# Optimization experiments

Hardware: AMD Instinct MI355X
Metric: run time of the kernel (lower is better)

The kernel has to match this reference:

```python
import jax, jax.numpy as jnp
import numpy as np

BITS = 4
GROUPSIZE = 128
IN_F = 4096
OUT_F = 11008
VALS_PER_I32 = 32 // BITS  # 8
MASK = (1 << BITS) - 1     # 0xF


def _dequant_weight(qweight, qzeros, scales):
    """GPTQ 4-bit dequant. qweight: [K//8, N] int32 packed along K;
    qzeros: [G, N//8] int32 packed along N; scales: [G, N].
    Returns float32 weight [K, N]."""
    shifts = (jnp.arange(VALS_PER_I32, dtype=jnp.uint32) * BITS)
    # unpack weights: each int32 row holds 8 consecutive K-rows
    qw = qweight.astype(jnp.uint32)                              # [K//8, N]
    w_int = ((qw[:, None, :] >> shifts[None, :, None]) & MASK)   # [K//8, 8, N]
    w_int = w_int.reshape(IN_F, OUT_F)                           # [K, N]
    # unpack zeros: each int32 col holds 8 consecutive N-cols; stored zeros = z - 1
    qz = qzeros.astype(jnp.uint32)                               # [G, N//8]
    z_int = ((qz[:, :, None] >> shifts[None, None, :]) & MASK)   # [G, N//8, 8]
    n_groups = qzeros.shape[0]
    z_int = z_int.reshape(n_groups, OUT_F) + 1                   # [G, N]
    # per-group dequant: w = scales[g] * (q - z[g])
    g_idx = jnp.arange(IN_F) // GROUPSIZE                        # [K]
    w = (w_int.astype(jnp.float32) - z_int.astype(jnp.float32)[g_idx]) * scales[g_idx]
    return w                                                     # [K, N]


def setup_inputs() -> dict:
    key = jax.random.key(0)
    k1, k2, k3, k4, k5 = jax.random.split(key, 5)
    n_groups = IN_F // GROUPSIZE
    x = jax.random.normal(k1, (4, IN_F), dtype=jnp.float32)
    scales = jax.random.uniform(k2, (n_groups, OUT_F), dtype=jnp.float32,
                                minval=0.001, maxval=0.01)
    bias = jax.random.normal(k3, (OUT_F,), dtype=jnp.float32)
    qweight = jax.random.randint(k4, (IN_F // 32 * BITS, OUT_F), 0, 2147483647,
                                 dtype=jnp.int32)
    qzeros = jax.random.randint(k5, (n_groups, OUT_F // 256 * (BITS * 8)), 0,
                                2147483647, dtype=jnp.int32)
    return {"x": x, "scales": scales, "bias": bias,
            "qweight": qweight, "qzeros": qzeros}


def reference(x, scales, bias, qweight, qzeros):
    w = _dequant_weight(qweight, qzeros, scales)    # [K, N] float32
    y = x.astype(jnp.float32) @ w + bias            # [tokens, N]
    return y.astype(x.dtype)
```

## Files before the change

### kernel.cpp

```cpp
#include <hip/hip_runtime.h>

#define IN_F 4096
#define OUT_F 11008
#define GROUPSIZE 128
#define NGROUPS 32
#define QROWS 512
#define ZCOLS 1376
#define KSPLIT 8
#define WS_FLOATS (KSPLIT * 4 * OUT_F)

__global__ __launch_bounds__(256) void gptq_partial_kernel(
    const float* __restrict__ x,
    const float* __restrict__ scales,
    const int*   __restrict__ qweight,
    const int*   __restrict__ qzeros,
    float*       __restrict__ ws)
{
    __shared__ float part[4][4][64];

    const int tid = threadIdx.x;
    const int col = tid & 63;
    const int kp  = tid >> 6;
    const int n   = blockIdx.x * 64 + col;
    const int g   = blockIdx.y * 4 + kp;
    const int gu  = __builtin_amdgcn_readfirstlane(g);

    const unsigned qz = (unsigned)qzeros[g * ZCOLS + (n >> 3)];
    const float zf = (float)(((qz >> (4u * (unsigned)(n & 7))) & 0xFu) + 1u);
    const float sc = scales[g * OUT_F + n];

    float ga[4] = {0.f, 0.f, 0.f, 0.f};
    const int kkbase = gu * (GROUPSIZE / 8);

    #pragma unroll
    for (int t = 0; t < GROUPSIZE / 8; ++t) {
        const int kk = kkbase + t;
        const unsigned w = (unsigned)qweight[kk * OUT_F + n];
        const unsigned lo = w & 0x0F0F0F0Fu;
        const unsigned hi = (w >> 4) & 0x0F0F0F0Fu;
        float q[8];
        q[0] = (float)(lo & 0xFFu);
        q[1] = (float)(hi & 0xFFu);
        q[2] = (float)((lo >> 8) & 0xFFu);
        q[3] = (float)((hi >> 8) & 0xFFu);
        q[4] = (float)((lo >> 16) & 0xFFu);
        q[5] = (float)((hi >> 16) & 0xFFu);
        q[6] = (float)((lo >> 24) & 0xFFu);
        q[7] = (float)((hi >> 24) & 0xFFu);

        const int k0 = kk * 8;
        #pragma unroll
        for (int j = 0; j < 8; ++j) {
            const float d = q[j] - zf;
            #pragma unroll
            for (int m = 0; m < 4; ++m) ga[m] += x[m * IN_F + k0 + j] * d;
        }
    }

    #pragma unroll
    for (int m = 0; m < 4; ++m) part[kp][m][col] = sc * ga[m];
    __syncthreads();

    const int m = tid >> 6;
    const int c = tid & 63;
    const int nn = blockIdx.x * 64 + c;
    const float s = part[0][m][c] + part[1][m][c] + part[2][m][c] + part[3][m][c];
    ws[(blockIdx.y * 4 + m) * OUT_F + nn] = s;
}

__global__ __launch_bounds__(256) void gptq_reduce_kernel(
    const float* __restrict__ ws,
    const float* __restrict__ bias,
    float*       __restrict__ out)
{
    const int n = blockIdx.x * 256 + threadIdx.x;
    const int m = blockIdx.y;
    float s = bias[n];
    #pragma unroll
    for (int ks = 0; ks < KSPLIT; ++ks)
        s += ws[(ks * 4 + m) * OUT_F + n];
    out[m * OUT_F + n] = s;
}

__global__ __launch_bounds__(256) void gptq_gemv_fused(
    const float* __restrict__ x, const float* __restrict__ scales,
    const float* __restrict__ bias, const int* __restrict__ qweight,
    const int* __restrict__ qzeros, float* __restrict__ out)
{
    __shared__ float part[4][4][64];
    const int tid = threadIdx.x;
    const int col = tid & 63;
    const int kp  = tid >> 6;
    const int n   = blockIdx.x * 64 + col;
    const unsigned zshift = 4u * (unsigned)(n & 7);
    const int zcol = n >> 3;
    float acc[4] = {0.f, 0.f, 0.f, 0.f};
    const int g0 = kp * (NGROUPS / 4);
    for (int g = g0; g < g0 + NGROUPS / 4; ++g) {
        const unsigned qz = (unsigned)qzeros[g * ZCOLS + zcol];
        const float zf = (float)(((qz >> zshift) & 0xFu) + 1u);
        const float sc = scales[g * OUT_F + n];
        float ga[4] = {0.f, 0.f, 0.f, 0.f};
        const int kkbase = g * (GROUPSIZE / 8);
        #pragma unroll 4
        for (int t = 0; t < GROUPSIZE / 8; ++t) {
            const int kk = kkbase + t;
            const unsigned w = (unsigned)qweight[kk * OUT_F + n];
            const unsigned lo = w & 0x0F0F0F0Fu;
            const unsigned hi = (w >> 4) & 0x0F0F0F0Fu;
            float q[8];
            q[0] = (float)(lo & 0xFFu);         q[1] = (float)(hi & 0xFFu);
            q[2] = (float)((lo >> 8) & 0xFFu);  q[3] = (float)((hi >> 8) & 0xFFu);
            q[4] = (float)((lo >> 16) & 0xFFu); q[5] = (float)((hi >> 16) & 0xFFu);
            q[6] = (float)((lo >> 24) & 0xFFu); q[7] = (float)((hi >> 24) & 0xFFu);
            const int k0 = kk * 8;
            #pragma unroll
            for (int j = 0; j < 8; ++j) {
                const float d = q[j] - zf;
                #pragma unroll
                for (int m = 0; m < 4; ++m) acc[m] += x[m * IN_F + k0 + j] * d * sc;
            }
        }
        (void)0;
    }
    #pragma unroll
    for (int m = 0; m < 4; ++m) part[kp][m][col] = acc[m];
    __syncthreads();
    const int m = tid >> 6;
    const int c = tid & 63;
    const int nn = blockIdx.x * 64 + c;
    const float s = part[0][m][c] + part[1][m][c] + part[2][m][c] + part[3][m][c];
    out[m * OUT_F + nn] = s + bias[nn];
}

extern "C" void kernel_launch(void* const* d_in, const int* in_sizes, int n_in,
                              void* d_out, int out_size, void* d_ws, size_t ws_size,
                              hipStream_t stream) {
    const float* x       = (const float*)d_in[0];
    const float* scales  = (const float*)d_in[1];
    const float* bias    = (const float*)d_in[2];
    const int*   qweight = (const int*)d_in[3];
    const int*   qzeros  = (const int*)d_in[4];
    float*       out     = (float*)d_out;

    if (ws_size >= WS_FLOATS * sizeof(float)) {
        float* ws = (float*)d_ws;
        dim3 g1(OUT_F / 64, KSPLIT);
        gptq_partial_kernel<<<g1, 256, 0, stream>>>(x, scales, qweight, qzeros, ws);
        dim3 g2(OUT_F / 256, 4);
        gptq_reduce_kernel<<<g2, 256, 0, stream>>>(ws, bias, out);
    } else {
        dim3 grid(OUT_F / 64);
        gptq_gemv_fused<<<grid, 256, 0, stream>>>(x, scales, bias, qweight, qzeros, out);
    }
}
```

Baseline: 16.84 us.

## Split GPTQ GEMV per group with int4 vector loads and packed-float math

Adds a new first stage in which each thread handles 4 adjacent output columns via int4 qweight loads and float4 scales. Each block covers one quantization group, split four ways in K across its waves, and the inner math uses 2-wide float vectors to allow packed FMA. Partials for all 32 groups go to a larger workspace, which a second kernel reduces with four independent accumulators. The change trades wider loads and more K-parallelism for more workspace traffic and a longer reduction. It falls back to the old paths when the workspace is too small.

```diff
diff --git a/kernel.cpp b/kernel.cpp
--- a/kernel.cpp
+++ b/kernel.cpp
@@ -1,4 +1,6 @@
 #include <hip/hip_runtime.h>
+
+typedef float v2f __attribute__((ext_vector_type(2)));
 
 #define IN_F 4096
 #define OUT_F 11008
@@ -6,32 +8,134 @@
 #define NGROUPS 32
 #define QROWS 512
 #define ZCOLS 1376
-#define KSPLIT 8
-#define WS_FLOATS (KSPLIT * 4 * OUT_F)
-
-__global__ __launch_bounds__(256) void gptq_partial_kernel(
+#define WS_NEW_BYTES ((size_t)NGROUPS * 4 * OUT_F * sizeof(float))
+#define WS_OLD_BYTES ((size_t)8 * 4 * OUT_F * sizeof(float))
+
+__global__ __launch_bounds__(256) void gptq_s1(
     const float* __restrict__ x,
     const float* __restrict__ scales,
     const int*   __restrict__ qweight,
     const int*   __restrict__ qzeros,
     float*       __restrict__ ws)
 {
+    __shared__ float part[4][4][256];
+
+    const int tid  = threadIdx.x;
+    const int lane = tid & 63;
+    const int kq   = __builtin_amdgcn_readfirstlane(tid >> 6);
+    const int c0   = blockIdx.x * 256 + lane * 4;
+    const int g    = blockIdx.y;
+
+    const unsigned qz  = (unsigned)qzeros[g * ZCOLS + (c0 >> 3)];
+    const unsigned zsh = 4u * (unsigned)(c0 & 7);
+    v2f zz[4];
+    #pragma unroll
+    for (int c = 0; c < 4; ++c) {
+        const float zf = (float)(((qz >> (zsh + 4u * c)) & 0xFu) + 1u);
+        zz[c].x = zf; zz[c].y = zf;
+    }
+
+    const float4 sc4 = *(const float4*)(scales + g * OUT_F + c0);
+
+    const int row0 = g * 16 + kq * 4;
+    v2f acc[4][4] = {};
+
+    #pragma unroll
+    for (int t = 0; t < 4; ++t) {
+        const int row = row0 + t;
+        const int4 w4 = *(const int4*)(qweight + row * OUT_F + c0);
+        const int k0  = row * 8;
+
+        v2f xp[4][4];
+        #pragma unroll
+        for (int m = 0; m < 4; ++m)
+            #pragma unroll
+            for (int jj = 0; jj < 4; ++jj)
+                xp[m][jj] = *(const v2f*)(x + m * IN_F + k0 + 2 * jj);
+
+        const unsigned wv[4] = {(unsigned)w4.x, (unsigned)w4.y,
+                                (unsigned)w4.z, (unsigned)w4.w};
+        #pragma unroll
+        for (int c = 0; c < 4; ++c) {
+            const unsigned w  = wv[c];
+            const unsigned lo = w & 0x0F0F0F0Fu;
+            const unsigned hi = (w >> 4) & 0x0F0F0F0Fu;
+            v2f d[4];
+            d[0].x = (float)(lo & 0xFFu);         d[0].y = (float)(hi & 0xFFu);
+            d[1].x = (float)((lo >> 8) & 0xFFu);  d[1].y = (float)((hi >> 8) & 0xFFu);
+            d[2].x = (float)((lo >> 16) & 0xFFu); d[2].y = (float)((hi >> 16) & 0xFFu);
+            d[3].x = (float)(lo >> 24);           d[3].y = (float)(hi >> 24);
+            #pragma unroll
+            for (int jj = 0; jj < 4; ++jj) d[jj] = d[jj] - zz[c];
+            #pragma unroll
+            for (int m = 0; m < 4; ++m) {
+                acc[m][c] += xp[m][0] * d[0];
+                acc[m][c] += xp[m][1] * d[1];
+                acc[m][c] += xp[m][2] * d[2];
+                acc[m][c] += xp[m][3] * d[3];
+            }
+        }
+    }
+
+    #pragma unroll
+    for (int m = 0; m < 4; ++m) {
+        float4 r;
+        r.x = (acc[m][0].x + acc[m][0].y) * sc4.x;
+        r.y = (acc[m][1].x + acc[m][1].y) * sc4.y;
+        r.z = (acc[m][2].x + acc[m][2].y) * sc4.z;
+        r.w = (acc[m][3].x + acc[m][3].y) * sc4.w;
+        *(float4*)&part[kq][m][lane * 4] = r;
+    }
+    __syncthreads();
+
+    const int m  = tid >> 6;
+    const int cc = (tid & 63) * 4;
+    float4 a = *(const float4*)&part[0][m][cc];
+    const float4 b = *(const float4*)&part[1][m][cc];
+    const float4 c2 = *(const float4*)&part[2][m][cc];
+    const float4 d2 = *(const float4*)&part[3][m][cc];
+    a.x += b.x + c2.x + d2.x;
+    a.y += b.y + c2.y + d2.y;
+    a.z += b.z + c2.z + d2.z;
+    a.w += b.w + c2.w + d2.w;
+    *(float4*)(ws + (g * 4 + m) * OUT_F + blockIdx.x * 256 + cc) = a;
+}
+
+__global__ __launch_bounds__(256) void gptq_s2(
+    const float* __restrict__ ws,
+    const float* __restrict__ bias,
+    float*       __restrict__ out)
+{
+    const int n = blockIdx.x * 256 + threadIdx.x;
+    const int m = blockIdx.y;
+    float s0 = bias[n], s1 = 0.f, s2 = 0.f, s3 = 0.f;
+    #pragma unroll
+    for (int g = 0; g < NGROUPS; g += 4) {
+        s0 += ws[((g + 0) * 4 + m) * OUT_F + n];
+        s1 += ws[((g + 1) * 4 + m) * OUT_F + n];
+        s2 += ws[((g + 2) * 4 + m) * OUT_F + n];
+        s3 += ws[((g + 3) * 4 + m) * OUT_F + n];
+    }
+    out[m * OUT_F + n] = (s0 + s1) + (s2 + s3);
+}
+
+__global__ __launch_bounds__(256) void gptq_partial_kernel(
+    const float* __restrict__ x, const float* __restrict__ scales,
+    const int* __restrict__ qweight, const int* __restrict__ qzeros,
+    float* __restrict__ ws)
+{
     __shared__ float part[4][4][64];
-
     const int tid = threadIdx.x;
     const int col = tid & 63;
     const int kp  = tid >> 6;
     const int n   = blockIdx.x * 64 + col;
     const int g   = blockIdx.y * 4 + kp;
     const int gu  = __builtin_amdgcn_readfirstlane(g);
-
     const unsigned qz = (unsigned)qzeros[g * ZCOLS + (n >> 3)];
     const float zf = (float)(((qz >> (4u * (unsigned)(n & 7))) & 0xFu) + 1u);
     const float sc = scales[g * OUT_F + n];
-
     float ga[4] = {0.f, 0.f, 0.f, 0.f};
     const int kkbase = gu * (GROUPSIZE / 8);
-
     #pragma unroll
     for (int t = 0; t < GROUPSIZE / 8; ++t) {
         const int kk = kkbase + t;
@@ -39,15 +143,10 @@
         const unsigned lo = w & 0x0F0F0F0Fu;
         const unsigned hi = (w >> 4) & 0x0F0F0F0Fu;
         float q[8];
-        q[0] = (float)(lo & 0xFFu);
-        q[1] = (float)(hi & 0xFFu);
-        q[2] = (float)((lo >> 8) & 0xFFu);
-        q[3] = (float)((hi >> 8) & 0xFFu);
-        q[4] = (float)((lo >> 16) & 0xFFu);
-        q[5] = (float)((hi >> 16) & 0xFFu);
-        q[6] = (float)((lo >> 24) & 0xFFu);
-        q[7] = (float)((hi >> 24) & 0xFFu);
-
+        q[0] = (float)(lo & 0xFFu);         q[1] = (float)(hi & 0xFFu);
+        q[2] = (float)((lo >> 8) & 0xFFu);  q[3] = (float)((hi >> 8) & 0xFFu);
+        q[4] = (float)((lo >> 16) & 0xFFu); q[5] = (float)((hi >> 16) & 0xFFu);
+        q[6] = (float)(lo >> 24);           q[7] = (float)(hi >> 24);
         const int k0 = kk * 8;
         #pragma unroll
         for (int j = 0; j < 8; ++j) {
@@ -56,11 +155,9 @@
             for (int m = 0; m < 4; ++m) ga[m] += x[m * IN_F + k0 + j] * d;
         }
     }
-
     #pragma unroll
     for (int m = 0; m < 4; ++m) part[kp][m][col] = sc * ga[m];
     __syncthreads();
-
     const int m = tid >> 6;
     const int c = tid & 63;
     const int nn = blockIdx.x * 64 + c;
@@ -69,16 +166,14 @@
 }
 
 __global__ __launch_bounds__(256) void gptq_reduce_kernel(
-    const float* __restrict__ ws,
-    const float* __restrict__ bias,
-    float*       __restrict__ out)
+    const float* __restrict__ ws, const float* __restrict__ bias,
+    float* __restrict__ out)
 {
     const int n = blockIdx.x * 256 + threadIdx.x;
     const int m = blockIdx.y;
     float s = bias[n];
     #pragma unroll
-    for (int ks = 0; ks < KSPLIT; ++ks)
-        s += ws[(ks * 4 + m) * OUT_F + n];
+    for (int ks = 0; ks < 8; ++ks) s += ws[(ks * 4 + m) * OUT_F + n];
     out[m * OUT_F + n] = s;
 }
 
@@ -95,16 +190,14 @@
     const unsigned zshift = 4u * (unsigned)(n & 7);
     const int zcol = n >> 3;
     float acc[4] = {0.f, 0.f, 0.f, 0.f};
-    const int g0 = kp * (NGROUPS / 4);
-    for (int g = g0; g < g0 + NGROUPS / 4; ++g) {
+    for (int g = kp * 8; g < kp * 8 + 8; ++g) {
         const unsigned qz = (unsigned)qzeros[g * ZCOLS + zcol];
         const float zf = (float)(((qz >> zshift) & 0xFu) + 1u);
         const float sc = scales[g * OUT_F + n];
         float ga[4] = {0.f, 0.f, 0.f, 0.f};
-        const int kkbase = g * (GROUPSIZE / 8);
         #pragma unroll 4
-        for (int t = 0; t < GROUPSIZE / 8; ++t) {
-            const int kk = kkbase + t;
+        for (int t = 0; t < 16; ++t) {
+            const int kk = g * 16 + t;
             const unsigned w = (unsigned)qweight[kk * OUT_F + n];
             const unsigned lo = w & 0x0F0F0F0Fu;
             const unsigned hi = (w >> 4) & 0x0F0F0F0Fu;
@@ -112,16 +205,17 @@
             q[0] = (float)(lo & 0xFFu);         q[1] = (float)(hi & 0xFFu);
             q[2] = (float)((lo >> 8) & 0xFFu);  q[3] = (float)((hi >> 8) & 0xFFu);
             q[4] = (float)((lo >> 16) & 0xFFu); q[5] = (float)((hi >> 16) & 0xFFu);
-            q[6] = (float)((lo >> 24) & 0xFFu); q[7] = (float)((hi >> 24) & 0xFFu);
+            q[6] = (float)(lo >> 24);           q[7] = (float)(hi >> 24);
             const int k0 = kk * 8;
             #pragma unroll
             for (int j = 0; j < 8; ++j) {
                 const float d = q[j] - zf;
                 #pragma unroll
-                for (int m = 0; m < 4; ++m) acc[m] += x[m * IN_F + k0 + j] * d * sc;
+                for (int m = 0; m < 4; ++m) ga[m] += x[m * IN_F + k0 + j] * d;
             }
         }
-        (void)0;
+        #pragma unroll
+        for (int m = 0; m < 4; ++m) acc[m] += sc * ga[m];
     }
     #pragma unroll
     for (int m = 0; m < 4; ++m) part[kp][m][col] = acc[m];
@@ -143,9 +237,15 @@
     const int*   qzeros  = (const int*)d_in[4];
     float*       out     = (float*)d_out;
 
-    if (ws_size >= WS_FLOATS * sizeof(float)) {
+    if (ws_size >= WS_NEW_BYTES) {
         float* ws = (float*)d_ws;
-        dim3 g1(OUT_F / 64, KSPLIT);
+        dim3 g1(OUT_F / 256, NGROUPS);
+        gptq_s1<<<g1, 256, 0, stream>>>(x, scales, qweight, qzeros, ws);
+        dim3 g2(OUT_F / 256, 4);
+        gptq_s2<<<g2, 256, 0, stream>>>(ws, bias, out);
+    } else if (ws_size >= WS_OLD_BYTES) {
+        float* ws = (float*)d_ws;
+        dim3 g1(OUT_F / 64, 8);
         gptq_partial_kernel<<<g1, 256, 0, stream>>>(x, scales, qweight, qzeros, ws);
         dim3 g2(OUT_F / 256, 4);
         gptq_reduce_kernel<<<g2, 256, 0, stream>>>(ws, bias, out);
```

Measured after the change: 17.92 us. 1.06x slower.

## Use bf16 MFMA for the split-K partial GEMV stage

Applied to the files above, without the earlier changes.

Replaces the scalar FMA partial kernel with one that dequantizes the 4-bit weights to bf16 and multiplies them by the activations with 16x16x32 bf16 MFMA. Activations are padded into rows 0-3 of the A operand, so 12 of the 16 MFMA rows carry zeros. The aim is to cut the VALU FMA cost of the dequant-multiply, at the price of bf16 precision for both x and the weights and a wasted share of MFMA throughput. The reduce kernel now uses two accumulators, and the fallback fused kernel applies scales once per group instead of on every FMA.

```diff
diff --git a/kernel.cpp b/kernel.cpp
--- a/kernel.cpp
+++ b/kernel.cpp
@@ -1,4 +1,7 @@
 #include <hip/hip_runtime.h>
+
+typedef short short8 __attribute__((ext_vector_type(8)));
+typedef float f32x4  __attribute__((ext_vector_type(4)));
 
 #define IN_F 4096
 #define OUT_F 11008
@@ -6,66 +9,77 @@
 #define NGROUPS 32
 #define QROWS 512
 #define ZCOLS 1376
-#define KSPLIT 8
-#define WS_FLOATS (KSPLIT * 4 * OUT_F)
+#define KSPL 8
+#define WS_BYTES ((size_t)KSPL * 4 * OUT_F * sizeof(float))
 
-__global__ __launch_bounds__(256) void gptq_partial_kernel(
+__device__ __forceinline__ unsigned cvt_pk_bf16(float a, float b) {
+    unsigned r;
+    asm("v_cvt_pk_bf16_f32 %0, %1, %2" : "=v"(r) : "v"(a), "v"(b));
+    return r;
+}
+
+__global__ __launch_bounds__(256) void gptq_s1_mfma(
     const float* __restrict__ x,
     const float* __restrict__ scales,
     const int*   __restrict__ qweight,
     const int*   __restrict__ qzeros,
     float*       __restrict__ ws)
 {
-    __shared__ float part[4][4][64];
+    const int tid  = threadIdx.x;
+    const int lane = tid & 63;
+    const int wv   = tid >> 6;
+    const int ks   = blockIdx.y;
+    const int ncol = lane & 15;
+    const int kb   = lane >> 4;
+    const int col  = blockIdx.x * 64 + wv * 16 + ncol;
 
-    const int tid = threadIdx.x;
-    const int col = tid & 63;
-    const int kp  = tid >> 6;
-    const int n   = blockIdx.x * 64 + col;
-    const int g   = blockIdx.y * 4 + kp;
-    const int gu  = __builtin_amdgcn_readfirstlane(g);
-
-    const unsigned qz = (unsigned)qzeros[g * ZCOLS + (n >> 3)];
-    const float zf = (float)(((qz >> (4u * (unsigned)(n & 7))) & 0xFu) + 1u);
-    const float sc = scales[g * OUT_F + n];
-
-    float ga[4] = {0.f, 0.f, 0.f, 0.f};
-    const int kkbase = gu * (GROUPSIZE / 8);
+    float tot[4] = {0.f, 0.f, 0.f, 0.f};
 
     #pragma unroll
-    for (int t = 0; t < GROUPSIZE / 8; ++t) {
-        const int kk = kkbase + t;
-        const unsigned w = (unsigned)qweight[kk * OUT_F + n];
-        const unsigned lo = w & 0x0F0F0F0Fu;
-        const unsigned hi = (w >> 4) & 0x0F0F0F0Fu;
-        float q[8];
-        q[0] = (float)(lo & 0xFFu);
-        q[1] = (float)(hi & 0xFFu);
-        q[2] = (float)((lo >> 8) & 0xFFu);
-        q[3] = (float)((hi >> 8) & 0xFFu);
-        q[4] = (float)((lo >> 16) & 0xFFu);
-        q[5] = (float)((hi >> 16) & 0xFFu);
-        q[6] = (float)((lo >> 24) & 0xFFu);
-        q[7] = (float)((hi >> 24) & 0xFFu);
+    for (int gi = 0; gi < 4; ++gi) {
+        const int g = ks * 4 + gi;
+        const unsigned qz = (unsigned)qzeros[g * ZCOLS + (col >> 3)];
+        const float z  = (float)(((qz >> (4u * (unsigned)(col & 7))) & 0xFu) + 1u);
+        const float sc = scales[g * OUT_F + col];
 
-        const int k0 = kk * 8;
+        f32x4 acc = {0.f, 0.f, 0.f, 0.f};
         #pragma unroll
-        for (int j = 0; j < 8; ++j) {
-            const float d = q[j] - zf;
-            #pragma unroll
-            for (int m = 0; m < 4; ++m) ga[m] += x[m * IN_F + k0 + j] * d;
+        for (int kt = 0; kt < 4; ++kt) {
+            const int k0  = g * GROUPSIZE + kt * 32;
+            const int row = (k0 >> 3) + kb;
+            const unsigned w = (unsigned)qweight[row * OUT_F + col];
+
+            const unsigned lo = w & 0x0F0F0F0Fu;
+            const unsigned hi = (w >> 4) & 0x0F0F0F0Fu;
+            union { unsigned u[4]; short8 s; } bf;
+            bf.u[0] = cvt_pk_bf16((float)(lo & 0xFFu) - z,         (float)(hi & 0xFFu) - z);
+            bf.u[1] = cvt_pk_bf16((float)((lo >> 8) & 0xFFu) - z,  (float)((hi >> 8) & 0xFFu) - z);
+            bf.u[2] = cvt_pk_bf16((float)((lo >> 16) & 0xFFu) - z, (float)((hi >> 16) & 0xFFu) - z);
+            bf.u[3] = cvt_pk_bf16((float)(lo >> 24) - z,           (float)(hi >> 24) - z);
+
+            union { unsigned u[4]; short8 s; } af;
+            af.u[0] = 0u; af.u[1] = 0u; af.u[2] = 0u; af.u[3] = 0u;
+            if (ncol < 4) {
+                const float* xp = x + ncol * IN_F + k0 + kb * 8;
+                const float4 xa = *(const float4*)xp;
+                const float4 xb = *(const float4*)(xp + 4);
+                af.u[0] = cvt_pk_bf16(xa.x, xa.y);
+                af.u[1] = cvt_pk_bf16(xa.z, xa.w);
+                af.u[2] = cvt_pk_bf16(xb.x, xb.y);
+                af.u[3] = cvt_pk_bf16(xb.z, xb.w);
+            }
+
+            acc = __builtin_amdgcn_mfma_f32_16x16x32_bf16(af.s, bf.s, acc, 0, 0, 0);
         }
+        #pragma unroll
+        for (int r = 0; r < 4; ++r) tot[r] += sc * acc[r];
     }
 
-    #pragma unroll
-    for (int m = 0; m < 4; ++m) part[kp][m][col] = sc * ga[m];
-    __syncthreads();
-
-    const int m = tid >> 6;
-    const int c = tid & 63;
-    const int nn = blockIdx.x * 64 + c;
-    const float s = part[0][m][c] + part[1][m][c] + part[2][m][c] + part[3][m][c];
-    ws[(blockIdx.y * 4 + m) * OUT_F + nn] = s;
+    if (lane < 16) {
+        #pragma unroll
+        for (int r = 0; r < 4; ++r)
+            ws[(size_t)(ks * 4 + r) * OUT_F + col] = tot[r];
+    }
 }
 
 __global__ __launch_bounds__(256) void gptq_reduce_kernel(
@@ -75,11 +89,13 @@
 {
     const int n = blockIdx.x * 256 + threadIdx.x;
     const int m = blockIdx.y;
-    float s = bias[n];
+    float s0 = bias[n], s1 = 0.f;
     #pragma unroll
-    for (int ks = 0; ks < KSPLIT; ++ks)
-        s += ws[(ks * 4 + m) * OUT_F + n];
-    out[m * OUT_F + n] = s;
+    for (int ks = 0; ks < KSPL; ks += 2) {
+        s0 += ws[(size_t)((ks + 0) * 4 + m) * OUT_F + n];
+        s1 += ws[(size_t)((ks + 1) * 4 + m) * OUT_F + n];
+    }
+    out[m * OUT_F + n] = s0 + s1;
 }
 
 __global__ __launch_bounds__(256) void gptq_gemv_fused(
@@ -95,16 +111,14 @@
     const unsigned zshift = 4u * (unsigned)(n & 7);
     const int zcol = n >> 3;
     float acc[4] = {0.f, 0.f, 0.f, 0.f};
-    const int g0 = kp * (NGROUPS / 4);
-    for (int g = g0; g < g0 + NGROUPS / 4; ++g) {
+    for (int g = kp * 8; g < kp * 8 + 8; ++g) {
         const unsigned qz = (unsigned)qzeros[g * ZCOLS + zcol];
         const float zf = (float)(((qz >> zshift) & 0xFu) + 1u);
         const float sc = scales[g * OUT_F + n];
         float ga[4] = {0.f, 0.f, 0.f, 0.f};
-        const int kkbase = g * (GROUPSIZE / 8);
         #pragma unroll 4
-        for (int t = 0; t < GROUPSIZE / 8; ++t) {
-            const int kk = kkbase + t;
+        for (int t = 0; t < 16; ++t) {
+            const int kk = g * 16 + t;
             const unsigned w = (unsigned)qweight[kk * OUT_F + n];
             const unsigned lo = w & 0x0F0F0F0Fu;
             const unsigned hi = (w >> 4) & 0x0F0F0F0Fu;
@@ -112,16 +126,17 @@
             q[0] = (float)(lo & 0xFFu);         q[1] = (float)(hi & 0xFFu);
             q[2] = (float)((lo >> 8) & 0xFFu);  q[3] = (float)((hi >> 8) & 0xFFu);
             q[4] = (float)((lo >> 16) & 0xFFu); q[5] = (float)((hi >> 16) & 0xFFu);
-            q[6] = (float)((lo >> 24) & 0xFFu); q[7] = (float)((hi >> 24) & 0xFFu);
+            q[6] = (float)(lo >> 24);           q[7] = (float)(hi >> 24);
             const int k0 = kk * 8;
             #pragma unroll
             for (int j = 0; j < 8; ++j) {
                 const float d = q[j] - zf;
                 #pragma unroll
-                for (int m = 0; m < 4; ++m) acc[m] += x[m * IN_F + k0 + j] * d * sc;
+                for (int m = 0; m < 4; ++m) ga[m] += x[m * IN_F + k0 + j] * d;
             }
         }
-        (void)0;
+        #pragma unroll
+        for (int m = 0; m < 4; ++m) acc[m] += sc * ga[m];
     }
     #pragma unroll
     for (int m = 0; m < 4; ++m) part[kp][m][col] = acc[m];
@@ -143,10 +158,10 @@
     const int*   qzeros  = (const int*)d_in[4];
     float*       out     = (float*)d_out;
 
-    if (ws_size >= WS_FLOATS * sizeof(float)) {
+    if (ws_size >= WS_BYTES) {
         float* ws = (float*)d_ws;
-        dim3 g1(OUT_F / 64, KSPLIT);
-        gptq_partial_kernel<<<g1, 256, 0, stream>>>(x, scales, qweight, qzeros, ws);
+        dim3 g1(OUT_F / 64, KSPL);
+        gptq_s1_mfma<<<g1, 256, 0, stream>>>(x, scales, qweight, qzeros, ws);
         dim3 g2(OUT_F / 256, 4);
         gptq_reduce_kernel<<<g2, 256, 0, stream>>>(ws, bias, out);
     } else {
```

New measurement: 20.63 us. 22.5% more time.
